# Kernel tuning notes

Measured on AMD Instinct MI355X. Metric: run time of the kernel, lower is better.

The kernel has to match this reference:

```python
import jax, jax.numpy as jnp
import numpy as np

BATCH = 1024


def setup_inputs() -> dict:
    key = jax.random.key(0)
    ks = jax.random.split(key, 8)
    piece_positions = jax.random.randint(ks[0], (BATCH, 64, 10), 0, 2) > 0  # bool occupancy
    king_positions = jax.random.randint(ks[1], (BATCH, 2), 0, 64, dtype=jnp.int32)
    input_weights = jax.random.randint(ks[2], (64, 641, 256), -32768, 32767, dtype=jnp.int16)
    input_bias = jnp.zeros((256,), dtype=jnp.int16)
    w1 = jax.random.randint(ks[3], (32, 512), -128, 127, dtype=jnp.int8)
    b1 = jnp.zeros((32,), dtype=jnp.int32)
    w2 = jax.random.randint(ks[4], (32, 32), -128, 127, dtype=jnp.int8)
    b2 = jnp.zeros((32,), dtype=jnp.int32)
    out_w = jax.random.randint(ks[5], (32,), -128, 127, dtype=jnp.int8)
    out_b = jnp.zeros((1,), dtype=jnp.int32)
    return {
        'piece_positions': piece_positions, 'king_positions': king_positions,
        'input_weights': input_weights, 'input_bias': input_bias,
        'w1': w1, 'b1': b1, 'w2': w2, 'b2': b2, 'out_w': out_w, 'out_b': out_b,
    }


def _fc(x, w, b):
    # int8 inputs/weights, int32 accumulate, floor-div 64, clamp to [0,127] -> int8
    y = x.astype(jnp.int32) @ w.T.astype(jnp.int32) + b
    y = jnp.floor_divide(y, 64)
    return jnp.clip(y, 0, 127).astype(jnp.int8)


def reference(piece_positions, king_positions, input_weights, input_bias,
              w1, b1, w2, b2, out_w, out_b):
    B = piece_positions.shape[0]
    pp = piece_positions.reshape(B, 640).astype(jnp.int32)  # flattened 64x10 HalfKP features

    def half(king_idx):
        wk = input_weights[king_idx]            # (B, 641, 256) gathered per-sample king table
        feats = wk[:, :640, :].astype(jnp.int32)
        kbias = wk[:, 640, :].astype(jnp.int32)
        return jnp.einsum('bf,bfd->bd', pp, feats) + kbias  # (B, 256)

    white = half(king_positions[:, 0])
    black = half(king_positions[:, 1])
    # int16 wraparound semantics of the original: accumulate in int32, mod-cast to int16
    acc = (white + black + input_bias.astype(jnp.int32)).astype(jnp.int16)

    x = jnp.clip(acc, 0, 127).astype(jnp.int8)
    x = jnp.concatenate([x, x], axis=1)  # (B, 512) side_to_move || other_side
    x = _fc(x, w1, b1)
    x = _fc(x, w2, b2)
    s = jnp.sum(x.astype(jnp.int32) * out_w.astype(jnp.int32)) + out_b  # scalar sum over batch too (as in source)
    return jnp.floor_divide(s, 16)  # shape (1,)
```

## Files before the change

### kernel.cpp

```cpp
#include <hip/hip_runtime.h>
#include <stdint.h>

#define NDIM  256
#define NFEAT 640
#define NROWS 641
#define SG    8
#define KCAP  2048
#define MAXSLOTS 2048
#define GRID_GATHER 1024
#define GRID_COMBINE 1024
#define OFF_KCNT  8
#define OFF_KLIST 128
#define OFF_PART  (OFF_KLIST + 64 * KCAP)

typedef unsigned short ushort4v __attribute__((ext_vector_type(4)));

struct FusedLds {
    union {
        unsigned mask[4][320];
        struct { alignas(16) int8_t x[NDIM]; int fc[256]; alignas(4) int8_t x2[32]; } c;
        int bcnt;
    };
};

__device__ __forceinline__ void detect_flags(const void* W, const void* pp,
                                             int* raww, int* rawpp)
{
    int a = 0, b = 0;
    const int* W32 = (const int*)W;
    const int* pp32 = (const int*)pp;
    for (int i = 0; i < 16; ++i) {
        const int v = W32[i];
        if (v > 32767 || v < -32768) a = 1;
        const int u = pp32[i];
        if (u != 0 && u != 1) b = 1;
    }
    *raww = a; *rawpp = b;
}

__global__ __launch_bounds__(256) void k_bucket(const int* __restrict__ kp,
                                                const void* __restrict__ W,
                                                const void* __restrict__ pp,
                                                int* __restrict__ ws, int nslots)
{
    __shared__ int bcnt;
    const int bid = blockIdx.x, t = threadIdx.x;
    int* kcnt  = ws + OFF_KCNT;
    int* klist = ws + OFF_KLIST;

    if (bid == 0 && t == 0) {
        int raww, rawpp;
        detect_flags(W, pp, &raww, &rawpp);
        ws[0] = 0; ws[1] = raww; ws[2] = rawpp; ws[3] = 0;
    }
    if (t == 0) bcnt = 0;
    __syncthreads();
    for (int s = t; s < nslots; s += 256) {
        if (kp[s] == bid) {
            const int pos = atomicAdd(&bcnt, 1);
            if (pos < KCAP) klist[bid * KCAP + pos] = s;
        }
    }
    __syncthreads();
    if (t == 0) kcnt[bid] = (bcnt > KCAP) ? KCAP : bcnt;
}

template<bool RAWW, bool RAWPP>
__device__ __forceinline__ void gather_phase(
    const void* __restrict__ ppv, const void* __restrict__ Wv,
    const int* __restrict__ kcnt, const int* __restrict__ klist,
    unsigned short* __restrict__ partial, int nslots, int rp,
    unsigned* __restrict__ maskbase)
{
    const int bid = blockIdx.x;
    const int k = bid & 63;
    const int t = threadIdx.x, l = t & 63, g = t >> 6;
    const int nwv = (gridDim.x >> 6) << 2;
    const int wv0 = ((bid >> 6) << 2) + g;
    unsigned* mym = maskbase + g * 320;

    const int cnt = kcnt[k];
    if (cnt <= 0) return;
    const int gmax = (cnt + SG - 1) >> 3;
    const int nunits = rp * gmax;
    const int rpb = NFEAT / rp;
    const int pshift = (rp == 16) ? 4 : (rp == 4) ? 2 : 1;
    const char* Wk = (const char*)Wv + (size_t)k * NROWS * NDIM * (RAWW ? 2 : 4);
    const int* kl = klist + k * KCAP;

    for (int u = wv0; u < nunits; u += nwv) {
        const int p = u & (rp - 1);
        const int gi = u >> pshift;
        const int base = gi * SG;
        const int ns = min(SG, cnt - base);
        const int r0 = p * rpb;

        int slots[SG], samps[SG];
        #pragma unroll
        for (int i = 0; i < SG; ++i) {
            const int s = kl[base + (i < ns ? i : ns - 1)];
            slots[i] = s; samps[i] = s >> 1;
        }

        for (int r = l; r < rpb; r += 64) {
            unsigned mm = 0;
            #pragma unroll
            for (int i = 0; i < SG; ++i) {
                int v;
                if (RAWPP) v = ((const uint8_t*)ppv)[(size_t)samps[i] * NFEAT + r0 + r];
                else       v = ((const int*)ppv)[(size_t)samps[i] * NFEAT + r0 + r];
                mm |= (v != 0 ? 1u : 0u) << i;
            }
            mym[r] = (ns < SG) ? (mm & ((1u << ns) - 1u)) : mm;
        }
        asm volatile("s_waitcnt lgkmcnt(0)" ::: "memory");

        ushort4v acc[SG];
        #pragma unroll
        for (int i = 0; i < SG; ++i) acc[i] = (ushort4v)0;

        const char* rb = Wk + (size_t)r0 * (RAWW ? 512 : 1024) + (size_t)l * (RAWW ? 8 : 16);
        const int rstep = RAWW ? 2048 : 4096;
        #pragma unroll 2
        for (int r = 0; r < rpb; r += 4, rb += rstep) {
            ushort4v w0, w1, w2, w3;
            if constexpr (RAWW) {
                w0 = *(const ushort4v*)(rb);
                w1 = *(const ushort4v*)(rb + 512);
                w2 = *(const ushort4v*)(rb + 1024);
                w3 = *(const ushort4v*)(rb + 1536);
            } else {
                const int4 u0 = *(const int4*)(rb);
                const int4 u1 = *(const int4*)(rb + 1024);
                const int4 u2 = *(const int4*)(rb + 2048);
                const int4 u3 = *(const int4*)(rb + 3072);
                w0.x=(unsigned short)u0.x; w0.y=(unsigned short)u0.y; w0.z=(unsigned short)u0.z; w0.w=(unsigned short)u0.w;
                w1.x=(unsigned short)u1.x; w1.y=(unsigned short)u1.y; w1.z=(unsigned short)u1.z; w1.w=(unsigned short)u1.w;
                w2.x=(unsigned short)u2.x; w2.y=(unsigned short)u2.y; w2.z=(unsigned short)u2.z; w2.w=(unsigned short)u2.w;
                w3.x=(unsigned short)u3.x; w3.y=(unsigned short)u3.y; w3.z=(unsigned short)u3.z; w3.w=(unsigned short)u3.w;
            }
            unsigned m0 = mym[r+0], m1 = mym[r+1], m2 = mym[r+2], m3 = mym[r+3];
            m0 = __builtin_amdgcn_readfirstlane(m0);
            m1 = __builtin_amdgcn_readfirstlane(m1);
            m2 = __builtin_amdgcn_readfirstlane(m2);
            m3 = __builtin_amdgcn_readfirstlane(m3);
            #pragma unroll
            for (int i = 0; i < SG; ++i) {
                if (m0 & (1u << i)) acc[i] += w0;
                if (m1 & (1u << i)) acc[i] += w1;
                if (m2 & (1u << i)) acc[i] += w2;
                if (m3 & (1u << i)) acc[i] += w3;
            }
        }

        #pragma unroll
        for (int i = 0; i < SG; ++i)
            if (i < ns)
                *(ushort4v*)&partial[((size_t)p * nslots + slots[i]) * NDIM + (size_t)l * 4] = acc[i];
    }
}

__global__ __launch_bounds__(256, 4) void k_gather(
    const void* __restrict__ pp, const void* __restrict__ W,
    int* __restrict__ ws, int nslots, int rp)
{
    __shared__ FusedLds sh;
    const int raww = ws[1], rawpp = ws[2];
    int* kcnt  = ws + OFF_KCNT;
    int* klist = ws + OFF_KLIST;
    unsigned short* partial = (unsigned short*)(ws + OFF_PART);
    if (raww) {
        if (rawpp) gather_phase<true,  true >(pp, W, kcnt, klist, partial, nslots, rp, &sh.mask[0][0]);
        else       gather_phase<true,  false>(pp, W, kcnt, klist, partial, nslots, rp, &sh.mask[0][0]);
    } else {
        if (rawpp) gather_phase<false, true >(pp, W, kcnt, klist, partial, nslots, rp, &sh.mask[0][0]);
        else       gather_phase<false, false>(pp, W, kcnt, klist, partial, nslots, rp, &sh.mask[0][0]);
    }
}

template<bool RAWW>
__device__ __forceinline__ void combine_phase(
    const unsigned short* __restrict__ partial, const int* __restrict__ kp,
    const void* __restrict__ Wv, const void* __restrict__ ibv,
    const void* __restrict__ w1v, const int* __restrict__ b1,
    const void* __restrict__ w2v, const int* __restrict__ b2,
    const void* __restrict__ owv, const int* __restrict__ ob,
    int* __restrict__ ws, int* __restrict__ out,
    int nslots, int B, int rp, FusedLds& sh)
{
    const int t = threadIdx.x;
    int blocksum = 0;

    for (int b = blockIdx.x; b < B; b += gridDim.x) {
        const int k0 = kp[2 * b + 0];
        const int k1 = kp[2 * b + 1];
        {
            unsigned tot = 0;
            for (int pi = 0; pi < rp; ++pi) {
                tot += partial[((size_t)pi * nslots + 2 * b + 0) * NDIM + t];
                tot += partial[((size_t)pi * nslots + 2 * b + 1) * NDIM + t];
            }
            if (RAWW) {
                const uint16_t* Wq = (const uint16_t*)Wv;
                tot += Wq[((size_t)k0 * NROWS + NFEAT) * NDIM + t];
                tot += Wq[((size_t)k1 * NROWS + NFEAT) * NDIM + t];
                tot += ((const uint16_t*)ibv)[t];
            } else {
                const int* Wq = (const int*)Wv;
                tot += (unsigned)Wq[((size_t)k0 * NROWS + NFEAT) * NDIM + t];
                tot += (unsigned)Wq[((size_t)k1 * NROWS + NFEAT) * NDIM + t];
                tot += (unsigned)((const int*)ibv)[t];
            }
            int v = (int)(int16_t)(uint16_t)tot;
            v = v < 0 ? 0 : (v > 127 ? 127 : v);
            sh.c.x[t] = (int8_t)v;
        }
        __syncthreads();

        {
            const int o = t >> 3, part = t & 7;
            int y = 0;
            const uint32_t* xw = (const uint32_t*)sh.c.x;
            if (RAWW) {
                const uint32_t* w1r = (const uint32_t*)((const char*)w1v + o * 512);
                #pragma unroll
                for (int i = 0; i < 8; ++i) {
                    const int wi = part * 8 + i;
                    const uint32_t xv = xw[wi];
                    const uint32_t wa = w1r[wi];
                    const uint32_t wb = w1r[64 + wi];
                    #pragma unroll
                    for (int jj = 0; jj < 4; ++jj) {
                        const int xj  = (int)((xv >> (8 * jj)) & 0xFFu);
                        const int waj = (int)(int8_t)(uint8_t)(wa >> (8 * jj));
                        const int wbj = (int)(int8_t)(uint8_t)(wb >> (8 * jj));
                        y += xj * (waj + wbj);
                    }
                }
            } else {
                const int* w1r = (const int*)w1v + o * 512;
                #pragma unroll
                for (int i = 0; i < 8; ++i) {
                    const int wi = part * 8 + i;
                    const uint32_t xv = xw[wi];
                    #pragma unroll
                    for (int jj = 0; jj < 4; ++jj) {
                        const int xj = (int)((xv >> (8 * jj)) & 0xFFu);
                        y += xj * (w1r[wi * 4 + jj] + w1r[256 + wi * 4 + jj]);
                    }
                }
            }
            sh.c.fc[t] = y;
        }
        __syncthreads();

        if (t < 32) {
            int y = b1[t];
            #pragma unroll
            for (int pq = 0; pq < 8; ++pq) y += sh.c.fc[t * 8 + pq];
            y >>= 6;
            y = y < 0 ? 0 : (y > 127 ? 127 : y);
            sh.c.x2[t] = (int8_t)y;
        }
        __syncthreads();

        if (t < 32) {
            int y = b2[t];
            const uint32_t* x2w = (const uint32_t*)sh.c.x2;
            if (RAWW) {
                const uint32_t* w2r = (const uint32_t*)((const char*)w2v + t * 32);
                #pragma unroll
                for (int i = 0; i < 8; ++i) {
                    const uint32_t xv = x2w[i];
                    const uint32_t wv = w2r[i];
                    #pragma unroll
                    for (int jj = 0; jj < 4; ++jj)
                        y += (int)((xv >> (8 * jj)) & 0xFFu) * (int)(int8_t)(uint8_t)(wv >> (8 * jj));
                }
            } else {
                const int* w2r = (const int*)w2v + t * 32;
                #pragma unroll
                for (int i = 0; i < 8; ++i) {
                    const uint32_t xv = x2w[i];
                    #pragma unroll
                    for (int jj = 0; jj < 4; ++jj)
                        y += (int)((xv >> (8 * jj)) & 0xFFu) * w2r[i * 4 + jj];
                }
            }
            y >>= 6;
            y = y < 0 ? 0 : (y > 127 ? 127 : y);
            const int owx = RAWW ? (int)((const int8_t*)owv)[t] : ((const int*)owv)[t];
            int pr = y * owx;
            #pragma unroll
            for (int off = 16; off > 0; off >>= 1) pr += __shfl_down(pr, off, 32);
            if (t == 0) blocksum += pr;
        }
        __syncthreads();
    }

    const int nticket = (int)gridDim.x < B ? (int)gridDim.x : B;
    if (t == 0 && (int)blockIdx.x < nticket) {
        atomicAdd(&ws[0], blocksum);
        __threadfence();
        const int ticket = atomicAdd(&ws[3], 1);
        if (ticket == nticket - 1) {
            const int s = atomicAdd(&ws[0], 0);
            out[0] = (s + ob[0]) >> 4;
        }
    }
}

__global__ __launch_bounds__(256) void k_combine(
    const int* __restrict__ kp, const void* __restrict__ W,
    const void* __restrict__ ib,
    const void* __restrict__ w1, const int* __restrict__ b1,
    const void* __restrict__ w2, const int* __restrict__ b2,
    const void* __restrict__ ow, const int* __restrict__ ob,
    int* __restrict__ ws, int* __restrict__ out, int nslots, int B, int rp)
{
    __shared__ FusedLds sh;
    unsigned short* partial = (unsigned short*)(ws + OFF_PART);
    if (ws[1]) combine_phase<true >(partial, kp, W, ib, w1, b1, w2, b2, ow, ob, ws, out, nslots, B, rp, sh);
    else       combine_phase<false>(partial, kp, W, ib, w1, b1, w2, b2, ow, ob, ws, out, nslots, B, rp, sh);
}

struct SharedBuf {
    uint8_t pp[NFEAT];
    int     acc[4][NDIM];
    alignas(16) int8_t x[NDIM];
    int     fc[256];
    alignas(4) int8_t x2[32];
    int     list[4][160];
};

__global__ void detect_layout(const int* __restrict__ W32, const int* __restrict__ pp32,
                              int* __restrict__ ws) {
    int raww, rawpp;
    detect_flags(W32, pp32, &raww, &rawpp);
    ws[0] = 0; ws[1] = raww; ws[2] = rawpp;
}

template<bool RAWW, bool RAWPP>
__device__ __forceinline__ void mono_body(
    const void* __restrict__ ppv, const int* __restrict__ kp,
    const void* __restrict__ Wv,  const void* __restrict__ ibv,
    const void* __restrict__ w1v, const int* __restrict__ b1,
    const void* __restrict__ w2v, const int* __restrict__ b2,
    const void* __restrict__ owv, int* __restrict__ ws, SharedBuf& sh)
{
    const int b = blockIdx.x;
    const int t = threadIdx.x;
    const int l = t & 63;
    const int g = t >> 6;

    if (RAWPP) {
        const uint32_t* src = (const uint32_t*)((const uint8_t*)ppv + (size_t)b * NFEAT);
        if (t < NFEAT / 4) ((uint32_t*)sh.pp)[t] = src[t];
    } else {
        const int* src = (const int*)ppv + (size_t)b * NFEAT;
        for (int i = t; i < NFEAT; i += 256) sh.pp[i] = (uint8_t)(src[i] != 0);
    }
    __syncthreads();

    const int base = g * 160;
    int cnt = 0;
    for (int c = 0; c < 160; c += 64) {
        const int idx = c + l;
        const bool flag = (idx < 160) && (sh.pp[base + idx] != 0);
        const unsigned long long mmask = __ballot(flag);
        const int pos = cnt + (int)__popcll(mmask & ((1ull << l) - 1ull));
        if (flag) sh.list[g][pos] = base + idx;
        cnt += (int)__popcll(mmask);
    }

    const int k0 = kp[b * 2 + 0];
    const int k1 = kp[b * 2 + 1];
    int a0 = 0, a1 = 0, a2 = 0, a3 = 0, a4 = 0, a5 = 0, a6 = 0, a7 = 0;

    if (RAWW) {
        const char* W0 = (const char*)Wv + (size_t)k0 * (NROWS * NDIM * 2);
        const char* W1 = (const char*)Wv + (size_t)k1 * (NROWS * NDIM * 2);
        const int lo = l * 8;
        auto step = [&](int f) {
            const uint2 u0 = *(const uint2*)(W0 + f * 512 + lo);
            const uint2 u1 = *(const uint2*)(W1 + f * 512 + lo);
            a0 += (int)(u0.x & 0xFFFFu); a1 += (int)(u0.x >> 16);
            a2 += (int)(u0.y & 0xFFFFu); a3 += (int)(u0.y >> 16);
            a4 += (int)(u1.x & 0xFFFFu); a5 += (int)(u1.x >> 16);
            a6 += (int)(u1.y & 0xFFFFu); a7 += (int)(u1.y >> 16);
        };
        int j = 0;
        for (; j + 4 <= cnt; j += 4) {
            const int f0 = sh.list[g][j], f1 = sh.list[g][j + 1];
            const int f2 = sh.list[g][j + 2], f3 = sh.list[g][j + 3];
            step(f0); step(f1); step(f2); step(f3);
        }
        for (; j < cnt; ++j) step(sh.list[g][j]);
    } else {
        const char* W0 = (const char*)Wv + (size_t)k0 * (NROWS * NDIM * 4);
        const char* W1 = (const char*)Wv + (size_t)k1 * (NROWS * NDIM * 4);
        const int lo = l * 16;
        auto step = [&](int f) {
            const int4 u0 = *(const int4*)(W0 + f * 1024 + lo);
            const int4 u1 = *(const int4*)(W1 + f * 1024 + lo);
            a0 += u0.x; a1 += u0.y; a2 += u0.z; a3 += u0.w;
            a4 += u1.x; a5 += u1.y; a6 += u1.z; a7 += u1.w;
        };
        int j = 0;
        for (; j + 4 <= cnt; j += 4) {
            const int f0 = sh.list[g][j], f1 = sh.list[g][j + 1];
            const int f2 = sh.list[g][j + 2], f3 = sh.list[g][j + 3];
            step(f0); step(f1); step(f2); step(f3);
        }
        for (; j < cnt; ++j) step(sh.list[g][j]);
    }

    sh.acc[g][4 * l + 0] = a0 + a4;
    sh.acc[g][4 * l + 1] = a1 + a5;
    sh.acc[g][4 * l + 2] = a2 + a6;
    sh.acc[g][4 * l + 3] = a3 + a7;
    __syncthreads();

    {
        const int d = t;
        int tot = sh.acc[0][d] + sh.acc[1][d] + sh.acc[2][d] + sh.acc[3][d];
        int kb0, kb1, ibx;
        if (RAWW) {
            const int16_t* Wq = (const int16_t*)Wv;
            kb0 = Wq[((size_t)k0 * NROWS + NFEAT) * NDIM + d];
            kb1 = Wq[((size_t)k1 * NROWS + NFEAT) * NDIM + d];
            ibx = ((const int16_t*)ibv)[d];
        } else {
            const int* Wq = (const int*)Wv;
            kb0 = Wq[((size_t)k0 * NROWS + NFEAT) * NDIM + d];
            kb1 = Wq[((size_t)k1 * NROWS + NFEAT) * NDIM + d];
            ibx = ((const int*)ibv)[d];
        }
        tot += kb0 + kb1 + ibx;
        int v = (int)(int16_t)(uint16_t)(uint32_t)tot;
        v = v < 0 ? 0 : (v > 127 ? 127 : v);
        sh.x[d] = (int8_t)v;
    }
    __syncthreads();

    {
        const int o = t >> 3, part = t & 7;
        int y = 0;
        const uint32_t* xw = (const uint32_t*)sh.x;
        if (RAWW) {
            const uint32_t* w1r = (const uint32_t*)((const char*)w1v + o * 512);
            #pragma unroll
            for (int i = 0; i < 8; ++i) {
                const int wi = part * 8 + i;
                const uint32_t xv = xw[wi];
                const uint32_t wa = w1r[wi];
                const uint32_t wb = w1r[64 + wi];
                #pragma unroll
                for (int jj = 0; jj < 4; ++jj) {
                    const int xj  = (int)((xv >> (8 * jj)) & 0xFFu);
                    const int waj = (int)(int8_t)(uint8_t)(wa >> (8 * jj));
                    const int wbj = (int)(int8_t)(uint8_t)(wb >> (8 * jj));
                    y += xj * (waj + wbj);
                }
            }
        } else {
            const int* w1r = (const int*)w1v + o * 512;
            #pragma unroll
            for (int i = 0; i < 8; ++i) {
                const int wi = part * 8 + i;
                const uint32_t xv = xw[wi];
                #pragma unroll
                for (int jj = 0; jj < 4; ++jj) {
                    const int xj = (int)((xv >> (8 * jj)) & 0xFFu);
                    y += xj * (w1r[wi * 4 + jj] + w1r[256 + wi * 4 + jj]);
                }
            }
        }
        sh.fc[t] = y;
    }
    __syncthreads();

    if (t < 32) {
        int y = b1[t];
        #pragma unroll
        for (int pq = 0; pq < 8; ++pq) y += sh.fc[t * 8 + pq];
        y >>= 6;
        y = y < 0 ? 0 : (y > 127 ? 127 : y);
        sh.x2[t] = (int8_t)y;
    }
    __syncthreads();

    if (t < 32) {
        int y = b2[t];
        const uint32_t* x2w = (const uint32_t*)sh.x2;
        if (RAWW) {
            const uint32_t* w2r = (const uint32_t*)((const char*)w2v + t * 32);
            #pragma unroll
            for (int i = 0; i < 8; ++i) {
                const uint32_t xv = x2w[i];
                const uint32_t wv = w2r[i];
                #pragma unroll
                for (int jj = 0; jj < 4; ++jj)
                    y += (int)((xv >> (8 * jj)) & 0xFFu) * (int)(int8_t)(uint8_t)(wv >> (8 * jj));
            }
        } else {
            const int* w2r = (const int*)w2v + t * 32;
            #pragma unroll
            for (int i = 0; i < 8; ++i) {
                const uint32_t xv = x2w[i];
                #pragma unroll
                for (int jj = 0; jj < 4; ++jj)
                    y += (int)((xv >> (8 * jj)) & 0xFFu) * w2r[i * 4 + jj];
            }
        }
        y >>= 6;
        y = y < 0 ? 0 : (y > 127 ? 127 : y);
        const int owx = RAWW ? (int)((const int8_t*)owv)[t] : ((const int*)owv)[t];
        int pr = y * owx;
        #pragma unroll
        for (int off = 16; off > 0; off >>= 1) pr += __shfl_down(pr, off, 32);
        if (t == 0) atomicAdd(ws, pr);
    }
}

__global__ __launch_bounds__(256, 4) void nnue_mono(
    const void* __restrict__ pp, const int* __restrict__ kp,
    const void* __restrict__ W,  const void* __restrict__ ib,
    const void* __restrict__ w1, const int* __restrict__ b1,
    const void* __restrict__ w2, const int* __restrict__ b2,
    const void* __restrict__ ow, int* __restrict__ ws)
{
    __shared__ SharedBuf sh;
    const int raww = ws[1], rawpp = ws[2];
    if (raww) {
        if (rawpp) mono_body<true,  true >(pp, kp, W, ib, w1, b1, w2, b2, ow, ws, sh);
        else       mono_body<true,  false>(pp, kp, W, ib, w1, b1, w2, b2, ow, ws, sh);
    } else {
        if (rawpp) mono_body<false, true >(pp, kp, W, ib, w1, b1, w2, b2, ow, ws, sh);
        else       mono_body<false, false>(pp, kp, W, ib, w1, b1, w2, b2, ow, ws, sh);
    }
}

__global__ void nnue_finalize(const int* __restrict__ ws, const int* __restrict__ ob,
                              int* __restrict__ out) {
    out[0] = (ws[0] + ob[0]) >> 4;
}

extern "C" void kernel_launch(void* const* d_in, const int* in_sizes, int n_in,
                              void* d_out, int out_size, void* d_ws, size_t ws_size,
                              hipStream_t stream)
{
    const void* pp = d_in[0];
    const int*  kp = (const int*)d_in[1];
    const void* W  = d_in[2];
    const void* ib = d_in[3];
    const void* w1 = d_in[4];
    const int*  b1 = (const int*)d_in[5];
    const void* w2 = d_in[6];
    const int*  b2 = (const int*)d_in[7];
    const void* ow = d_in[8];
    const int*  ob = (const int*)d_in[9];
    int* ws  = (int*)d_ws;
    int* out = (int*)d_out;

    const int B = in_sizes[1] / 2;
    const int nslots = 2 * B;

    const size_t need16 = ((size_t)OFF_PART + (size_t)16 * nslots * (NDIM / 2)) * 4;
    const size_t need4  = ((size_t)OFF_PART + (size_t) 4 * nslots * (NDIM / 2)) * 4;
    const size_t need2  = ((size_t)OFF_PART + (size_t) 2 * nslots * (NDIM / 2)) * 4;
    int rp = 0;
    if (ws_size >= need16)     rp = 16;
    else if (ws_size >= need4) rp = 4;
    else if (ws_size >= need2) rp = 2;

    if (rp && nslots <= MAXSLOTS && B > 0) {
        hipLaunchKernelGGL(k_bucket, dim3(64), dim3(256), 0, stream,
                           kp, W, pp, ws, nslots);
        hipLaunchKernelGGL(k_gather, dim3(GRID_GATHER), dim3(256), 0, stream,
                           pp, W, ws, nslots, rp);
        hipLaunchKernelGGL(k_combine, dim3(GRID_COMBINE), dim3(256), 0, stream,
                           kp, W, ib, w1, b1, w2, b2, ow, ob, ws, out, nslots, B, rp);
        return;
    }

    hipLaunchKernelGGL(detect_layout, dim3(1), dim3(1), 0, stream,
                       (const int*)W, (const int*)pp, ws);
    hipLaunchKernelGGL(nnue_mono, dim3(B), dim3(256), 0, stream,
                       pp, kp, W, ib, w1, b1, w2, b2, ow, ws);
    hipLaunchKernelGGL(nnue_finalize, dim3(1), dim3(1), 0, stream, ws, ob, out);
}
```

Measured before the change: 156.1 us.

## Keep feature masks in registers, batch weight loads, vectorize combine partial reduction

When a row partition has at most 64 rows, the gather phase keeps each lane's occupancy mask in a register and broadcasts it with readlane, skipping the LDS round trip. It also loads eight weight rows per iteration instead of four. The combine phase now reads partials as 4-wide vectors, with the rp partitions split across the four waves and reduced through LDS. The threadfence before the ticket atomic becomes a vmcnt wait. These changes aim to cut LDS traffic, raise memory-level parallelism and widen loads, at the cost of more registers and an extra barrier.

```diff
diff --git a/kernel.cpp b/kernel.cpp
--- a/kernel.cpp
+++ b/kernel.cpp
@@ -15,12 +15,15 @@
 
 typedef unsigned short ushort4v __attribute__((ext_vector_type(4)));
 
-struct FusedLds {
-    union {
-        unsigned mask[4][320];
-        struct { alignas(16) int8_t x[NDIM]; int fc[256]; alignas(4) int8_t x2[32]; } c;
-        int bcnt;
-    };
+struct GatherLds {
+    unsigned mask[4][320];
+};
+
+struct CombineLds {
+    alignas(16) int8_t x[NDIM];
+    int fc[256];
+    alignas(4) int8_t x2[32];
+    alignas(16) ushort4v red[4][64];
 };
 
 __device__ __forceinline__ void detect_flags(const void* W, const void* pp,
@@ -85,6 +88,7 @@
     const int nunits = rp * gmax;
     const int rpb = NFEAT / rp;
     const int pshift = (rp == 16) ? 4 : (rp == 4) ? 2 : 1;
+    const int rowb = RAWW ? 512 : 1024;
     const char* Wk = (const char*)Wv + (size_t)k * NROWS * NDIM * (RAWW ? 2 : 4);
     const int* kl = klist + k * KCAP;
 
@@ -93,6 +97,7 @@
         const int gi = u >> pshift;
         const int base = gi * SG;
         const int ns = min(SG, cnt - base);
+        const unsigned emask = (ns < SG) ? ((1u << ns) - 1u) : 0xFFu;
         const int r0 = p * rpb;
 
         int slots[SG], samps[SG];
@@ -102,54 +107,86 @@
             slots[i] = s; samps[i] = s >> 1;
         }
 
-        for (int r = l; r < rpb; r += 64) {
-            unsigned mm = 0;
-            #pragma unroll
-            for (int i = 0; i < SG; ++i) {
-                int v;
-                if (RAWPP) v = ((const uint8_t*)ppv)[(size_t)samps[i] * NFEAT + r0 + r];
-                else       v = ((const int*)ppv)[(size_t)samps[i] * NFEAT + r0 + r];
-                mm |= (v != 0 ? 1u : 0u) << i;
-            }
-            mym[r] = (ns < SG) ? (mm & ((1u << ns) - 1u)) : mm;
-        }
-        asm volatile("s_waitcnt lgkmcnt(0)" ::: "memory");
-
         ushort4v acc[SG];
         #pragma unroll
         for (int i = 0; i < SG; ++i) acc[i] = (ushort4v)0;
 
-        const char* rb = Wk + (size_t)r0 * (RAWW ? 512 : 1024) + (size_t)l * (RAWW ? 8 : 16);
-        const int rstep = RAWW ? 2048 : 4096;
-        #pragma unroll 2
-        for (int r = 0; r < rpb; r += 4, rb += rstep) {
-            ushort4v w0, w1, w2, w3;
-            if constexpr (RAWW) {
-                w0 = *(const ushort4v*)(rb);
-                w1 = *(const ushort4v*)(rb + 512);
-                w2 = *(const ushort4v*)(rb + 1024);
-                w3 = *(const ushort4v*)(rb + 1536);
-            } else {
-                const int4 u0 = *(const int4*)(rb);
-                const int4 u1 = *(const int4*)(rb + 1024);
-                const int4 u2 = *(const int4*)(rb + 2048);
-                const int4 u3 = *(const int4*)(rb + 3072);
-                w0.x=(unsigned short)u0.x; w0.y=(unsigned short)u0.y; w0.z=(unsigned short)u0.z; w0.w=(unsigned short)u0.w;
-                w1.x=(unsigned short)u1.x; w1.y=(unsigned short)u1.y; w1.z=(unsigned short)u1.z; w1.w=(unsigned short)u1.w;
-                w2.x=(unsigned short)u2.x; w2.y=(unsigned short)u2.y; w2.z=(unsigned short)u2.z; w2.w=(unsigned short)u2.w;
-                w3.x=(unsigned short)u3.x; w3.y=(unsigned short)u3.y; w3.z=(unsigned short)u3.z; w3.w=(unsigned short)u3.w;
-            }
-            unsigned m0 = mym[r+0], m1 = mym[r+1], m2 = mym[r+2], m3 = mym[r+3];
-            m0 = __builtin_amdgcn_readfirstlane(m0);
-            m1 = __builtin_amdgcn_readfirstlane(m1);
-            m2 = __builtin_amdgcn_readfirstlane(m2);
-            m3 = __builtin_amdgcn_readfirstlane(m3);
-            #pragma unroll
-            for (int i = 0; i < SG; ++i) {
-                if (m0 & (1u << i)) acc[i] += w0;
-                if (m1 & (1u << i)) acc[i] += w1;
-                if (m2 & (1u << i)) acc[i] += w2;
-                if (m3 & (1u << i)) acc[i] += w3;
+        if (rpb <= 64) {
+            unsigned mm = 0;
+            if (l < rpb) {
+                #pragma unroll
+                for (int i = 0; i < SG; ++i) {
+                    int v;
+                    if (RAWPP) v = ((const uint8_t*)ppv)[(size_t)samps[i] * NFEAT + r0 + l];
+                    else       v = ((const int*)ppv)[(size_t)samps[i] * NFEAT + r0 + l];
+                    mm |= (v != 0 ? 1u : 0u) << i;
+                }
+                mm &= emask;
+            }
+            const char* rb = Wk + (size_t)r0 * rowb + (size_t)l * (RAWW ? 8 : 16);
+            for (int r = 0; r < rpb; r += 8, rb += 8 * rowb) {
+                ushort4v w[8];
+                #pragma unroll
+                for (int j = 0; j < 8; ++j) {
+                    if constexpr (RAWW) {
+                        w[j] = *(const ushort4v*)(rb + j * 512);
+                    } else {
+                        const int4 u4 = *(const int4*)(rb + j * 1024);
+                        w[j].x = (unsigned short)u4.x; w[j].y = (unsigned short)u4.y;
+                        w[j].z = (unsigned short)u4.z; w[j].w = (unsigned short)u4.w;
+                    }
+                }
+                #pragma unroll
+                for (int j = 0; j < 8; ++j) {
+                    const unsigned m = (unsigned)__builtin_amdgcn_readlane((int)mm, r + j);
+                    #pragma unroll
+                    for (int i = 0; i < SG; ++i)
+                        if (m & (1u << i)) acc[i] += w[j];
+                }
+            }
+        } else {
+            for (int r = l; r < rpb; r += 64) {
+                unsigned mm = 0;
+                #pragma unroll
+                for (int i = 0; i < SG; ++i) {
+                    int v;
+                    if (RAWPP) v = ((const uint8_t*)ppv)[(size_t)samps[i] * NFEAT + r0 + r];
+                    else       v = ((const int*)ppv)[(size_t)samps[i] * NFEAT + r0 + r];
+                    mm |= (v != 0 ? 1u : 0u) << i;
+                }
+                mym[r] = mm & emask;
+            }
+            asm volatile("s_waitcnt lgkmcnt(0)" ::: "memory");
+
+            const char* rb = Wk + (size_t)r0 * rowb + (size_t)l * (RAWW ? 8 : 16);
+            for (int r = 0; r < rpb; r += 4, rb += 4 * rowb) {
+                ushort4v w0, w1, w2, w3;
+                if constexpr (RAWW) {
+                    w0 = *(const ushort4v*)(rb);
+                    w1 = *(const ushort4v*)(rb + 512);
+                    w2 = *(const ushort4v*)(rb + 1024);
+                    w3 = *(const ushort4v*)(rb + 1536);
+                } else {
+                    const int4 u0 = *(const int4*)(rb);
+                    const int4 u1 = *(const int4*)(rb + 1024);
+                    const int4 u2 = *(const int4*)(rb + 2048);
+                    const int4 u3 = *(const int4*)(rb + 3072);
+                    w0.x=(unsigned short)u0.x; w0.y=(unsigned short)u0.y; w0.z=(unsigned short)u0.z; w0.w=(unsigned short)u0.w;
+                    w1.x=(unsigned short)u1.x; w1.y=(unsigned short)u1.y; w1.z=(unsigned short)u1.z; w1.w=(unsigned short)u1.w;
+                    w2.x=(unsigned short)u2.x; w2.y=(unsigned short)u2.y; w2.z=(unsigned short)u2.z; w2.w=(unsigned short)u2.w;
+                    w3.x=(unsigned short)u3.x; w3.y=(unsigned short)u3.y; w3.z=(unsigned short)u3.z; w3.w=(unsigned short)u3.w;
+                }
+                unsigned m0 = __builtin_amdgcn_readfirstlane(mym[r+0]);
+                unsigned m1 = __builtin_amdgcn_readfirstlane(mym[r+1]);
+                unsigned m2 = __builtin_amdgcn_readfirstlane(mym[r+2]);
+                unsigned m3 = __builtin_amdgcn_readfirstlane(mym[r+3]);
+                #pragma unroll
+                for (int i = 0; i < SG; ++i) {
+                    if (m0 & (1u << i)) acc[i] += w0;
+                    if (m1 & (1u << i)) acc[i] += w1;
+                    if (m2 & (1u << i)) acc[i] += w2;
+                    if (m3 & (1u << i)) acc[i] += w3;
+                }
             }
         }
 
@@ -164,7 +201,7 @@
     const void* __restrict__ pp, const void* __restrict__ W,
     int* __restrict__ ws, int nslots, int rp)
 {
-    __shared__ FusedLds sh;
+    __shared__ GatherLds sh;
     const int raww = ws[1], rawpp = ws[2];
     int* kcnt  = ws + OFF_KCNT;
     int* klist = ws + OFF_KLIST;
@@ -186,41 +223,54 @@
     const void* __restrict__ w2v, const int* __restrict__ b2,
     const void* __restrict__ owv, const int* __restrict__ ob,
     int* __restrict__ ws, int* __restrict__ out,
-    int nslots, int B, int rp, FusedLds& sh)
-{
-    const int t = threadIdx.x;
+    int nslots, int B, int rp, CombineLds& sh)
+{
+    const int t = threadIdx.x, l = t & 63, g = t >> 6;
     int blocksum = 0;
 
     for (int b = blockIdx.x; b < B; b += gridDim.x) {
         const int k0 = kp[2 * b + 0];
         const int k1 = kp[2 * b + 1];
+
         {
-            unsigned tot = 0;
-            for (int pi = 0; pi < rp; ++pi) {
-                tot += partial[((size_t)pi * nslots + 2 * b + 0) * NDIM + t];
-                tot += partial[((size_t)pi * nslots + 2 * b + 1) * NDIM + t];
-            }
+            ushort4v a4 = (ushort4v)0;
+            for (int pi = g; pi < rp; pi += 4) {
+                a4 += *(const ushort4v*)&partial[((size_t)pi * nslots + 2 * b + 0) * NDIM + 4 * l];
+                a4 += *(const ushort4v*)&partial[((size_t)pi * nslots + 2 * b + 1) * NDIM + 4 * l];
+            }
+            sh.red[g][l] = a4;
+        }
+        __syncthreads();
+        if (t < 64) {
+            ushort4v tot = sh.red[0][l] + sh.red[1][l] + sh.red[2][l] + sh.red[3][l];
             if (RAWW) {
                 const uint16_t* Wq = (const uint16_t*)Wv;
-                tot += Wq[((size_t)k0 * NROWS + NFEAT) * NDIM + t];
-                tot += Wq[((size_t)k1 * NROWS + NFEAT) * NDIM + t];
-                tot += ((const uint16_t*)ibv)[t];
+                tot += *(const ushort4v*)&Wq[((size_t)k0 * NROWS + NFEAT) * NDIM + 4 * l];
+                tot += *(const ushort4v*)&Wq[((size_t)k1 * NROWS + NFEAT) * NDIM + 4 * l];
+                tot += *(const ushort4v*)&((const uint16_t*)ibv)[4 * l];
             } else {
                 const int* Wq = (const int*)Wv;
-                tot += (unsigned)Wq[((size_t)k0 * NROWS + NFEAT) * NDIM + t];
-                tot += (unsigned)Wq[((size_t)k1 * NROWS + NFEAT) * NDIM + t];
-                tot += (unsigned)((const int*)ibv)[t];
-            }
-            int v = (int)(int16_t)(uint16_t)tot;
-            v = v < 0 ? 0 : (v > 127 ? 127 : v);
-            sh.c.x[t] = (int8_t)v;
+                const int4 kb0 = *(const int4*)&Wq[((size_t)k0 * NROWS + NFEAT) * NDIM + 4 * l];
+                const int4 kb1 = *(const int4*)&Wq[((size_t)k1 * NROWS + NFEAT) * NDIM + 4 * l];
+                const int4 ib4 = *(const int4*)&((const int*)ibv)[4 * l];
+                tot.x += (unsigned short)(kb0.x + kb1.x + ib4.x);
+                tot.y += (unsigned short)(kb0.y + kb1.y + ib4.y);
+                tot.z += (unsigned short)(kb0.z + kb1.z + ib4.z);
+                tot.w += (unsigned short)(kb0.w + kb1.w + ib4.w);
+            }
+            #pragma unroll
+            for (int j = 0; j < 4; ++j) {
+                int v = (int)(int16_t)(uint16_t)tot[j];
+                v = v < 0 ? 0 : (v > 127 ? 127 : v);
+                sh.x[4 * l + j] = (int8_t)v;
+            }
         }
         __syncthreads();
 
         {
             const int o = t >> 3, part = t & 7;
             int y = 0;
-            const uint32_t* xw = (const uint32_t*)sh.c.x;
+            const uint32_t* xw = (const uint32_t*)sh.x;
             if (RAWW) {
                 const uint32_t* w1r = (const uint32_t*)((const char*)w1v + o * 512);
                 #pragma unroll
@@ -250,23 +300,23 @@
                     }
                 }
             }
-            sh.c.fc[t] = y;
+            sh.fc[t] = y;
         }
         __syncthreads();
 
         if (t < 32) {
             int y = b1[t];
             #pragma unroll
-            for (int pq = 0; pq < 8; ++pq) y += sh.c.fc[t * 8 + pq];
+            for (int pq = 0; pq < 8; ++pq) y += sh.fc[t * 8 + pq];
             y >>= 6;
             y = y < 0 ? 0 : (y > 127 ? 127 : y);
-            sh.c.x2[t] = (int8_t)y;
+            sh.x2[t] = (int8_t)y;
         }
         __syncthreads();
 
         if (t < 32) {
             int y = b2[t];
-            const uint32_t* x2w = (const uint32_t*)sh.c.x2;
+            const uint32_t* x2w = (const uint32_t*)sh.x2;
             if (RAWW) {
                 const uint32_t* w2r = (const uint32_t*)((const char*)w2v + t * 32);
                 #pragma unroll
@@ -301,7 +351,7 @@
     const int nticket = (int)gridDim.x < B ? (int)gridDim.x : B;
     if (t == 0 && (int)blockIdx.x < nticket) {
         atomicAdd(&ws[0], blocksum);
-        __threadfence();
+        asm volatile("s_waitcnt vmcnt(0)" ::: "memory");
         const int ticket = atomicAdd(&ws[3], 1);
         if (ticket == nticket - 1) {
             const int s = atomicAdd(&ws[0], 0);
@@ -318,7 +368,7 @@
     const void* __restrict__ ow, const int* __restrict__ ob,
     int* __restrict__ ws, int* __restrict__ out, int nslots, int B, int rp)
 {
-    __shared__ FusedLds sh;
+    __shared__ CombineLds sh;
     unsigned short* partial = (unsigned short*)(ws + OFF_PART);
     if (ws[1]) combine_phase<true >(partial, kp, W, ib, w1, b1, w2, b2, ow, ob, ws, out, nslots, B, rp, sh);
     else       combine_phase<false>(partial, kp, W, ib, w1, b1, w2, b2, ow, ob, ws, out, nslots, B, rp, sh);
```

Measured after the change: 152.0 us. 2.6% less time.
